# Kernel tuning notes

Hardware: AMD Instinct MI355X
Metric: run time of the kernel (lower is better)

## Reference

```python
import jax, jax.numpy as jnp
import numpy as np

HEADS = 16
HEAD_DIM = 64

def setup_inputs() -> dict:
    key = jax.random.key(0)
    ks = jax.random.split(key, 5)
    S, B, H = 1024, 4, 1024
    scale = 1.0 / np.sqrt(H)
    return {
        "hidden_states": jax.random.normal(ks[0], (S, B, H), jnp.float32),
        "attention_mask": jnp.zeros((B * HEADS, 1, S), jnp.float32),
        "Wq": jax.random.normal(ks[1], (H, H), jnp.float32) * scale,
        "bq": jnp.zeros((H,), jnp.float32),
        "Wk": jax.random.normal(ks[2], (H, H), jnp.float32) * scale,
        "bk": jnp.zeros((H,), jnp.float32),
        "Wv": jax.random.normal(ks[3], (H, H), jnp.float32) * scale,
        "bv": jnp.zeros((H,), jnp.float32),
    }

def reference(hidden_states, attention_mask, Wq, bq, Wk, bk, Wv, bv):
    S, B, H = hidden_states.shape
    d = HEAD_DIM
    inv_sqrt_d = 1.0 / np.sqrt(d)
    # QKV projections (torch Linear: x @ W.T + b)
    q = hidden_states @ Wq.T + bq  # (S, B, H)
    k = hidden_states @ Wk.T + bk
    v = hidden_states @ Wv.T + bv
    # (S, B*heads, d) -> (B*heads, S, d)
    q = q.reshape(S, B * HEADS, d).transpose(1, 0, 2)
    k = k.reshape(S, B * HEADS, d).transpose(1, 0, 2)
    v = v.reshape(S, B * HEADS, d).transpose(1, 0, 2)
    # SDDMM: scaled scores + additive mask -> (B*heads, S, S)
    scores = jnp.einsum('nsd,ntd->nst', q, k) * inv_sqrt_d + attention_mask
    probs = jax.nn.softmax(scores, axis=-1)
    # AV bmm -> (B*heads, S, d); note: dropout in source is seeded but never applied
    ctx = jnp.einsum('nst,ntd->nsd', probs, v)
    # back to (S, B, hidden)
    ctx = ctx.transpose(1, 0, 2).reshape(S, B, H)
    return ctx
```

## Files before the change

kernel.cpp:

```cpp
#include <hip/hip_runtime.h>
#include <hip/hip_bf16.h>
#include <math.h>

#define S_LEN 1024
#define BATCH 4
#define HID 1024
#define NHEADS 16
#define DHEAD 64
#define NTOT 64
#define M_ROWS 4096

typedef unsigned short u16;
typedef unsigned int u32;
typedef __bf16 bf16x8 __attribute__((ext_vector_type(8)));
typedef float f32x4 __attribute__((ext_vector_type(4)));

__device__ __forceinline__ u16 f2bf(float x) {
    __hip_bfloat16 h = __float2bfloat16(x);
    return *(u16*)&h;
}

__device__ __forceinline__ float fexp2(float x) {
#if __has_builtin(__builtin_amdgcn_exp2f)
    return __builtin_amdgcn_exp2f(x);
#else
    return __expf(x * 0.6931471805599453f);
#endif
}

__device__ __forceinline__ u32 cvtpk(float a, float b) {
    u32 r;
    asm("v_cvt_pk_bf16_f32 %0, %1, %2" : "=v"(r) : "v"(a), "v"(b));
    return r;
}

__device__ __forceinline__ void pl16swap(u32& a, u32& b) {
    asm("v_permlane16_swap_b32 %0, %1" : "+v"(a), "+v"(b));
}

__device__ __forceinline__ void gll16(const u16* g, u16* l) {
    __builtin_amdgcn_global_load_lds(
        (const __attribute__((address_space(1))) u32*)g,
        (__attribute__((address_space(3))) u32*)l, 16, 0, 0);
}

__global__ __launch_bounds__(256) void cvt_all(
    const float* __restrict__ X, const float* __restrict__ wq,
    const float* __restrict__ wk, const float* __restrict__ wv,
    u16* __restrict__ Xb, u16* __restrict__ Wb)
{
    const int bid = blockIdx.x;
    const float* src;
    u16* dst;
    size_t off;
    if (bid < 4096) {
        src = X; dst = Xb; off = (size_t)bid * 1024;
    } else {
        const int wb = bid - 4096;
        const int which = wb >> 10;
        src = (which == 0) ? wq : (which == 1) ? wk : wv;
        dst = Wb + (size_t)which * HID * HID;
        off = (size_t)(wb & 1023) * 1024;
    }
    const size_t idx = off + threadIdx.x * 4;
    float4 x = *(const float4*)(src + idx);
    *(ushort4*)(dst + idx) = make_ushort4(f2bf(x.x), f2bf(x.y), f2bf(x.z), f2bf(x.w));
}

__global__ __launch_bounds__(256, 3) void qkv_mfma(
    const u16* __restrict__ Xb, const u16* __restrict__ Wb,
    const float* __restrict__ bq, const float* __restrict__ bk,
    const float* __restrict__ bv,
    u16* __restrict__ Qb, u16* __restrict__ Kb, u16* __restrict__ VT)
{
    const int m0 = blockIdx.x * 128;
    const int n0 = blockIdx.y * 128;
    const int which = blockIdx.z;

    __shared__ __align__(16) u16 As[128 * 64];
    __shared__ __align__(16) u16 Bs[128 * 64];

    const int tid = threadIdx.x;
    const int lane = tid & 63;
    const int w = tid >> 6;
    const int wm = w & 1, wn = w >> 1;
    const int quad = lane >> 4;
    const int l15 = lane & 15;
    const int r7 = l15 & 7;

    const u16* W = Wb + (size_t)which * HID * HID;

    f32x4 acc[4][4];
    #pragma unroll
    for (int i = 0; i < 4; ++i)
        #pragma unroll
        for (int j = 0; j < 4; ++j)
            #pragma unroll
            for (int r = 0; r < 4; ++r) acc[i][j][r] = 0.0f;

    const int srow = lane >> 3;
    const int scg  = ((lane & 7) ^ srow) * 8;

    for (int k0 = 0; k0 < HID; k0 += 64) {
        #pragma unroll
        for (int c = 0; c < 4; ++c) {
            const int seg = w * 4 + c;
            const int row = seg * 8 + srow;
            gll16(Xb + (size_t)(m0 + row) * HID + k0 + scg, As + seg * 512);
            gll16(W  + (size_t)(n0 + row) * HID + k0 + scg, Bs + seg * 512);
        }
        __syncthreads();

        #pragma unroll
        for (int kk = 0; kk < 2; ++kk) {
            const int xo = ((kk * 4 + quad) ^ r7) * 8;
            bf16x8 af[4], bf[4];
            #pragma unroll
            for (int i = 0; i < 4; ++i)
                af[i] = *(const bf16x8*)(As + (wm * 64 + i * 16 + l15) * 64 + xo);
            #pragma unroll
            for (int j = 0; j < 4; ++j)
                bf[j] = *(const bf16x8*)(Bs + (wn * 64 + j * 16 + l15) * 64 + xo);
            #pragma unroll
            for (int i = 0; i < 4; ++i)
                #pragma unroll
                for (int j = 0; j < 4; ++j)
                    acc[i][j] = __builtin_amdgcn_mfma_f32_16x16x32_bf16(
                        af[i], bf[j], acc[i][j], 0, 0, 0);
        }
        __syncthreads();
    }

    const float* bias = (which == 0) ? bq : (which == 1) ? bk : bv;
    #pragma unroll
    for (int j = 0; j < 4; ++j) {
        const int o = n0 + wn * 64 + j * 16 + l15;
        const float bias_v = bias[o];
        const int head = o >> 6, d = o & 63;
        #pragma unroll
        for (int i = 0; i < 4; ++i) {
            const int mbase = m0 + wm * 64 + i * 16 + quad * 4;
            const int s = mbase >> 2;
            #pragma unroll
            for (int r = 0; r < 4; ++r) {
                const int n = r * NHEADS + head;
                const u16 hv = f2bf(acc[i][j][r] + bias_v);
                if (which == 0)
                    Qb[((size_t)n * S_LEN + s) * DHEAD + d] = hv;
                else if (which == 1)
                    Kb[((size_t)n * S_LEN + s) * DHEAD + d] = hv;
                else
                    VT[(size_t)n * (DHEAD * S_LEN) + (size_t)d * S_LEN + s] = hv;
            }
        }
    }
}

__global__ __launch_bounds__(256, 2) void attn_mfma(
    const u16* __restrict__ Qb, const u16* __restrict__ Kb,
    const u16* __restrict__ VT, const float* __restrict__ mask,
    float* __restrict__ out)
{
    const int bid = blockIdx.x;
    const int swz = (bid & 7) * 64 + (bid >> 3);
    const int n = swz >> 3;
    const int s0 = (swz & 7) * 128;
    const int b = n >> 4, head = n & 15;

    __shared__ __align__(16) char smem[36864];
    u16* Kbuf = (u16*)smem;
    u16* Vbuf = (u16*)(smem + 16384);
    float* Ms = (float*)(smem + 32768);
    float* Of = (float*)smem;

    const int tid = threadIdx.x;
    const int lane = tid & 63;
    const int w = tid >> 6;
    const int quad = lane >> 4;
    const int l15 = lane & 15;
    const int r7 = l15 & 7;
    const size_t nbase = (size_t)n * S_LEN * DHEAD;

    const float LOG2E = 1.44269504f;
    const float SCL2  = 0.18033688f;
    const float MOFF  = -23.0831099f;

    const int xs0 = ((quad ^ r7) * 8);
    const int xs1 = (((4 + quad) ^ r7) * 8);
    const int qperm = ((quad & 1) << 1) | (quad >> 1);
    const int xv0 = ((qperm ^ r7) * 8);
    const int xv1 = (((4 + qperm) ^ r7) * 8);

    const int srow = lane >> 3;
    const int scg  = (lane & 7) ^ (srow & 7);

    {
        float4 mv = *(const float4*)(mask + (size_t)n * S_LEN + tid * 4);
        Ms[tid * 4 + 0] = fmaf(mv.x, LOG2E, MOFF);
        Ms[tid * 4 + 1] = fmaf(mv.y, LOG2E, MOFF);
        Ms[tid * 4 + 2] = fmaf(mv.z, LOG2E, MOFF);
        Ms[tid * 4 + 3] = fmaf(mv.w, LOG2E, MOFF);
    }

    bf16x8 qf[2][2];
    #pragma unroll
    for (int mi = 0; mi < 2; ++mi)
        #pragma unroll
        for (int st = 0; st < 2; ++st)
            qf[mi][st] = *(const bf16x8*)(Qb + nbase +
                (size_t)(s0 + w * 32 + mi * 16 + l15) * 64 + st * 32 + quad * 8);

    f32x4 O[2][4];
    float l_lane[2];
    #pragma unroll
    for (int mi = 0; mi < 2; ++mi) {
        l_lane[mi] = 0.0f;
        #pragma unroll
        for (int jt = 0; jt < 4; ++jt)
            #pragma unroll
            for (int r = 0; r < 4; ++r) O[mi][jt][r] = 0.0f;
    }

    {
        #pragma unroll
        for (int c = 0; c < 2; ++c) {
            const int seg = w * 2 + c;
            const int row = seg * 8 + srow;
            gll16(Kb + nbase + (size_t)row * 64 + scg * 8, Kbuf + seg * 512);
            gll16(VT + nbase + (size_t)row * S_LEN + scg * 8, Vbuf + seg * 512);
        }
    }
    __syncthreads();

    for (int it = 0; it < 16; ++it) {
        const int t0 = it * 64;
        const u16* kb = Kbuf + (it & 1) * 4096;
        const u16* vb = Vbuf + (it & 1) * 4096;

        if (it < 15) {
            u16* kd = Kbuf + ((it + 1) & 1) * 4096;
            u16* vd = Vbuf + ((it + 1) & 1) * 4096;
            #pragma unroll
            for (int c = 0; c < 2; ++c) {
                const int seg = w * 2 + c;
                const int row = seg * 8 + srow;
                gll16(Kb + nbase + (size_t)(t0 + 64 + row) * 64 + scg * 8, kd + seg * 512);
                gll16(VT + nbase + (size_t)row * S_LEN + t0 + 64 + scg * 8, vd + seg * 512);
            }
        }

        f32x4 sc[2][4];
        #pragma unroll
        for (int mi = 0; mi < 2; ++mi)
            #pragma unroll
            for (int j = 0; j < 4; ++j)
                #pragma unroll
                for (int r = 0; r < 4; ++r) sc[mi][j][r] = 0.0f;

        __builtin_amdgcn_s_setprio(1);
        #pragma unroll
        for (int st = 0; st < 2; ++st) {
            const int xo = st ? xs1 : xs0;
            bf16x8 kf[4];
            #pragma unroll
            for (int j = 0; j < 4; ++j)
                kf[j] = *(const bf16x8*)(kb + (j * 16 + l15) * 64 + xo);
            #pragma unroll
            for (int mi = 0; mi < 2; ++mi)
                #pragma unroll
                for (int j = 0; j < 4; ++j)
                    sc[mi][j] = __builtin_amdgcn_mfma_f32_16x16x32_bf16(
                        kf[j], qf[mi][st], sc[mi][j], 0, 0, 0);
        }
        __builtin_amdgcn_s_setprio(0);

        float4 mb4[4];
        #pragma unroll
        for (int j = 0; j < 4; ++j)
            mb4[j] = *(const float4*)(Ms + t0 + j * 16 + quad * 4);

        u32 pw[2][2][4];
        #pragma unroll
        for (int mi = 0; mi < 2; ++mi) {
            float pj[4][4];
            #pragma unroll
            for (int j = 0; j < 4; ++j) {
                pj[j][0] = fexp2(fmaf(sc[mi][j][0], SCL2, mb4[j].x));
                pj[j][1] = fexp2(fmaf(sc[mi][j][1], SCL2, mb4[j].y));
                pj[j][2] = fexp2(fmaf(sc[mi][j][2], SCL2, mb4[j].z));
                pj[j][3] = fexp2(fmaf(sc[mi][j][3], SCL2, mb4[j].w));
                l_lane[mi] += (pj[j][0] + pj[j][1]) + (pj[j][2] + pj[j][3]);
            }
            u32 W00 = cvtpk(pj[0][0], pj[0][1]), W01 = cvtpk(pj[0][2], pj[0][3]);
            u32 W10 = cvtpk(pj[1][0], pj[1][1]), W11 = cvtpk(pj[1][2], pj[1][3]);
            u32 W20 = cvtpk(pj[2][0], pj[2][1]), W21 = cvtpk(pj[2][2], pj[2][3]);
            u32 W30 = cvtpk(pj[3][0], pj[3][1]), W31 = cvtpk(pj[3][2], pj[3][3]);
            pl16swap(W00, W10); pl16swap(W01, W11);
            pl16swap(W20, W30); pl16swap(W21, W31);
            pw[mi][0][0] = W00; pw[mi][0][1] = W01;
            pw[mi][0][2] = W10; pw[mi][0][3] = W11;
            pw[mi][1][0] = W20; pw[mi][1][1] = W21;
            pw[mi][1][2] = W30; pw[mi][1][3] = W31;
        }

        __builtin_amdgcn_s_setprio(1);
        #pragma unroll
        for (int st = 0; st < 2; ++st) {
            const int xo = st ? xv1 : xv0;
            bf16x8 vf[4];
            #pragma unroll
            for (int jt = 0; jt < 4; ++jt)
                vf[jt] = *(const bf16x8*)(vb + (jt * 16 + l15) * 64 + xo);
            #pragma unroll
            for (int mi = 0; mi < 2; ++mi) {
                union { u32 wds[4]; bf16x8 v; } pu;
                pu.wds[0] = pw[mi][st][0]; pu.wds[1] = pw[mi][st][1];
                pu.wds[2] = pw[mi][st][2]; pu.wds[3] = pw[mi][st][3];
                #pragma unroll
                for (int jt = 0; jt < 4; ++jt)
                    O[mi][jt] = __builtin_amdgcn_mfma_f32_16x16x32_bf16(
                        vf[jt], pu.v, O[mi][jt], 0, 0, 0);
            }
        }
        __builtin_amdgcn_s_setprio(0);

        __syncthreads();
    }

    float inv_l[2];
    #pragma unroll
    for (int mi = 0; mi < 2; ++mi) {
        float l = l_lane[mi];
        l += __shfl_xor(l, 16);
        l += __shfl_xor(l, 32);
        inv_l[mi] = 1.0f / l;
    }
    __syncthreads();

    #pragma unroll
    for (int mi = 0; mi < 2; ++mi) {
        const int q = w * 32 + mi * 16 + l15;
        #pragma unroll
        for (int jt = 0; jt < 4; ++jt)
            #pragma unroll
            for (int r = 0; r < 4; ++r)
                Of[q * 72 + jt * 16 + quad * 4 + r] = O[mi][jt][r] * inv_l[mi];
    }
    __syncthreads();

    const int tx = tid & 15, ty = tid >> 4;
    #pragma unroll
    for (int p = 0; p < 8; ++p) {
        const int q = p * 16 + ty;
        float4 v = *(const float4*)(Of + q * 72 + tx * 4);
        *(float4*)(out + (size_t)(s0 + q) * (BATCH * HID) + (size_t)b * HID +
                   head * DHEAD + tx * 4) = v;
    }
}

extern "C" void kernel_launch(void* const* d_in, const int* in_sizes, int n_in,
                              void* d_out, int out_size, void* d_ws, size_t ws_size,
                              hipStream_t stream)
{
    const float* X    = (const float*)d_in[0];
    const float* mask = (const float*)d_in[1];
    const float* Wq   = (const float*)d_in[2];
    const float* bq   = (const float*)d_in[3];
    const float* Wk   = (const float*)d_in[4];
    const float* bk   = (const float*)d_in[5];
    const float* Wv   = (const float*)d_in[6];
    const float* bv   = (const float*)d_in[7];
    float* out = (float*)d_out;

    const size_t MX = (size_t)M_ROWS * HID;
    const size_t MW = (size_t)HID * HID;
    u16* wsp = (u16*)d_ws;
    u16* Xb = wsp;
    u16* Wb = Xb + MX;
    u16* Qb = Wb + 3 * MW;
    u16* Kb = Qb + MX;
    u16* VT = Kb + MX;

    cvt_all<<<dim3(4096 + 3072), 256, 0, stream>>>(X, Wq, Wk, Wv, Xb, Wb);
    qkv_mfma<<<dim3(M_ROWS / 128, HID / 128, 3), 256, 0, stream>>>(
        Xb, Wb, bq, bk, bv, Qb, Kb, VT);
    attn_mfma<<<dim3(S_LEN / 128 * NTOT), 256, 0, stream>>>(Qb, Kb, VT, mask, out);
}
```

Baseline: 146.5 us.

## Process 128-key tiles per iteration to halve barrier count in attention loop

The attention kernel's KV loop now covers 128 keys per iteration as two 64-key halves instead of one 64-key tile, with double-buffered K/V shared memory doubled to 64 KB. This halves the number of __syncthreads barriers and async-load rounds. The two halves' exp/pack results are held in registers before the PV MFMAs. The larger LDS footprint (about 68 KB per block) and extra live registers may reduce occupancy below the 2 blocks per CU requested in launch bounds.

```diff
diff --git a/kernel.cpp b/kernel.cpp
--- a/kernel.cpp
+++ b/kernel.cpp
@@ -167,10 +167,10 @@
     const int s0 = (swz & 7) * 128;
     const int b = n >> 4, head = n & 15;
 
-    __shared__ __align__(16) char smem[36864];
+    __shared__ __align__(16) char smem[69632];
     u16* Kbuf = (u16*)smem;
-    u16* Vbuf = (u16*)(smem + 16384);
-    float* Ms = (float*)(smem + 32768);
+    u16* Vbuf = (u16*)(smem + 32768);
+    float* Ms = (float*)(smem + 65536);
     float* Of = (float*)smem;
 
     const int tid = threadIdx.x;
@@ -223,103 +223,124 @@
 
     {
         #pragma unroll
-        for (int c = 0; c < 2; ++c) {
-            const int seg = w * 2 + c;
-            const int row = seg * 8 + srow;
-            gll16(Kb + nbase + (size_t)row * 64 + scg * 8, Kbuf + seg * 512);
-            gll16(VT + nbase + (size_t)row * S_LEN + scg * 8, Vbuf + seg * 512);
-        }
-    }
-    __syncthreads();
-
-    for (int it = 0; it < 16; ++it) {
-        const int t0 = it * 64;
-        const u16* kb = Kbuf + (it & 1) * 4096;
-        const u16* vb = Vbuf + (it & 1) * 4096;
-
-        if (it < 15) {
-            u16* kd = Kbuf + ((it + 1) & 1) * 4096;
-            u16* vd = Vbuf + ((it + 1) & 1) * 4096;
+        for (int h = 0; h < 2; ++h) {
             #pragma unroll
             for (int c = 0; c < 2; ++c) {
                 const int seg = w * 2 + c;
                 const int row = seg * 8 + srow;
-                gll16(Kb + nbase + (size_t)(t0 + 64 + row) * 64 + scg * 8, kd + seg * 512);
-                gll16(VT + nbase + (size_t)row * S_LEN + t0 + 64 + scg * 8, vd + seg * 512);
-            }
-        }
-
-        f32x4 sc[2][4];
-        #pragma unroll
-        for (int mi = 0; mi < 2; ++mi)
+                gll16(Kb + nbase + (size_t)(h * 64 + row) * 64 + scg * 8,
+                      Kbuf + h * 4096 + seg * 512);
+                gll16(VT + nbase + (size_t)row * S_LEN + h * 64 + scg * 8,
+                      Vbuf + h * 4096 + seg * 512);
+            }
+        }
+    }
+    __syncthreads();
+
+    u32 pw[2][2][2][4];
+
+    for (int it = 0; it < 8; ++it) {
+        const int t0 = it * 128;
+        const u16* kb = Kbuf + (it & 1) * 8192;
+        const u16* vb = Vbuf + (it & 1) * 8192;
+
+        if (it < 7) {
+            u16* kd = Kbuf + ((it + 1) & 1) * 8192;
+            u16* vd = Vbuf + ((it + 1) & 1) * 8192;
+            const int t0n = t0 + 128;
+            #pragma unroll
+            for (int h = 0; h < 2; ++h) {
+                #pragma unroll
+                for (int c = 0; c < 2; ++c) {
+                    const int seg = w * 2 + c;
+                    const int row = seg * 8 + srow;
+                    gll16(Kb + nbase + (size_t)(t0n + h * 64 + row) * 64 + scg * 8,
+                          kd + h * 4096 + seg * 512);
+                    gll16(VT + nbase + (size_t)row * S_LEN + t0n + h * 64 + scg * 8,
+                          vd + h * 4096 + seg * 512);
+                }
+            }
+        }
+
+        #pragma unroll
+        for (int h = 0; h < 2; ++h) {
+            const u16* kbh = kb + h * 4096;
+
+            f32x4 sc[2][4];
+            #pragma unroll
+            for (int mi = 0; mi < 2; ++mi)
+                #pragma unroll
+                for (int j = 0; j < 4; ++j)
+                    #pragma unroll
+                    for (int r = 0; r < 4; ++r) sc[mi][j][r] = 0.0f;
+
+            __builtin_amdgcn_s_setprio(1);
+            #pragma unroll
+            for (int st = 0; st < 2; ++st) {
+                const int xo = st ? xs1 : xs0;
+                bf16x8 kf[4];
+                #pragma unroll
+                for (int j = 0; j < 4; ++j)
+                    kf[j] = *(const bf16x8*)(kbh + (j * 16 + l15) * 64 + xo);
+                #pragma unroll
+                for (int mi = 0; mi < 2; ++mi)
+                    #pragma unroll
+                    for (int j = 0; j < 4; ++j)
+                        sc[mi][j] = __builtin_amdgcn_mfma_f32_16x16x32_bf16(
+                            kf[j], qf[mi][st], sc[mi][j], 0, 0, 0);
+            }
+            __builtin_amdgcn_s_setprio(0);
+
+            float4 mb4[4];
             #pragma unroll
             for (int j = 0; j < 4; ++j)
-                #pragma unroll
-                for (int r = 0; r < 4; ++r) sc[mi][j][r] = 0.0f;
+                mb4[j] = *(const float4*)(Ms + t0 + h * 64 + j * 16 + quad * 4);
+
+            #pragma unroll
+            for (int mi = 0; mi < 2; ++mi) {
+                float pj[4][4];
+                #pragma unroll
+                for (int j = 0; j < 4; ++j) {
+                    pj[j][0] = fexp2(fmaf(sc[mi][j][0], SCL2, mb4[j].x));
+                    pj[j][1] = fexp2(fmaf(sc[mi][j][1], SCL2, mb4[j].y));
+                    pj[j][2] = fexp2(fmaf(sc[mi][j][2], SCL2, mb4[j].z));
+                    pj[j][3] = fexp2(fmaf(sc[mi][j][3], SCL2, mb4[j].w));
+                    l_lane[mi] += (pj[j][0] + pj[j][1]) + (pj[j][2] + pj[j][3]);
+                }
+                u32 W00 = cvtpk(pj[0][0], pj[0][1]), W01 = cvtpk(pj[0][2], pj[0][3]);
+                u32 W10 = cvtpk(pj[1][0], pj[1][1]), W11 = cvtpk(pj[1][2], pj[1][3]);
+                u32 W20 = cvtpk(pj[2][0], pj[2][1]), W21 = cvtpk(pj[2][2], pj[2][3]);
+                u32 W30 = cvtpk(pj[3][0], pj[3][1]), W31 = cvtpk(pj[3][2], pj[3][3]);
+                pl16swap(W00, W10); pl16swap(W01, W11);
+                pl16swap(W20, W30); pl16swap(W21, W31);
+                pw[mi][h][0][0] = W00; pw[mi][h][0][1] = W01;
+                pw[mi][h][0][2] = W10; pw[mi][h][0][3] = W11;
+                pw[mi][h][1][0] = W20; pw[mi][h][1][1] = W21;
+                pw[mi][h][1][2] = W30; pw[mi][h][1][3] = W31;
+            }
+        }
 
         __builtin_amdgcn_s_setprio(1);
         #pragma unroll
-        for (int st = 0; st < 2; ++st) {
-            const int xo = st ? xs1 : xs0;
-            bf16x8 kf[4];
-            #pragma unroll
-            for (int j = 0; j < 4; ++j)
-                kf[j] = *(const bf16x8*)(kb + (j * 16 + l15) * 64 + xo);
-            #pragma unroll
-            for (int mi = 0; mi < 2; ++mi)
-                #pragma unroll
-                for (int j = 0; j < 4; ++j)
-                    sc[mi][j] = __builtin_amdgcn_mfma_f32_16x16x32_bf16(
-                        kf[j], qf[mi][st], sc[mi][j], 0, 0, 0);
-        }
-        __builtin_amdgcn_s_setprio(0);
-
-        float4 mb4[4];
-        #pragma unroll
-        for (int j = 0; j < 4; ++j)
-            mb4[j] = *(const float4*)(Ms + t0 + j * 16 + quad * 4);
-
-        u32 pw[2][2][4];
-        #pragma unroll
-        for (int mi = 0; mi < 2; ++mi) {
-            float pj[4][4];
-            #pragma unroll
-            for (int j = 0; j < 4; ++j) {
-                pj[j][0] = fexp2(fmaf(sc[mi][j][0], SCL2, mb4[j].x));
-                pj[j][1] = fexp2(fmaf(sc[mi][j][1], SCL2, mb4[j].y));
-                pj[j][2] = fexp2(fmaf(sc[mi][j][2], SCL2, mb4[j].z));
-                pj[j][3] = fexp2(fmaf(sc[mi][j][3], SCL2, mb4[j].w));
-                l_lane[mi] += (pj[j][0] + pj[j][1]) + (pj[j][2] + pj[j][3]);
-            }
-            u32 W00 = cvtpk(pj[0][0], pj[0][1]), W01 = cvtpk(pj[0][2], pj[0][3]);
-            u32 W10 = cvtpk(pj[1][0], pj[1][1]), W11 = cvtpk(pj[1][2], pj[1][3]);
-            u32 W20 = cvtpk(pj[2][0], pj[2][1]), W21 = cvtpk(pj[2][2], pj[2][3]);
-            u32 W30 = cvtpk(pj[3][0], pj[3][1]), W31 = cvtpk(pj[3][2], pj[3][3]);
-            pl16swap(W00, W10); pl16swap(W01, W11);
-            pl16swap(W20, W30); pl16swap(W21, W31);
-            pw[mi][0][0] = W00; pw[mi][0][1] = W01;
-            pw[mi][0][2] = W10; pw[mi][0][3] = W11;
-            pw[mi][1][0] = W20; pw[mi][1][1] = W21;
-            pw[mi][1][2] = W30; pw[mi][1][3] = W31;
-        }
-
-        __builtin_amdgcn_s_setprio(1);
-        #pragma unroll
-        for (int st = 0; st < 2; ++st) {
-            const int xo = st ? xv1 : xv0;
-            bf16x8 vf[4];
-            #pragma unroll
-            for (int jt = 0; jt < 4; ++jt)
-                vf[jt] = *(const bf16x8*)(vb + (jt * 16 + l15) * 64 + xo);
-            #pragma unroll
-            for (int mi = 0; mi < 2; ++mi) {
-                union { u32 wds[4]; bf16x8 v; } pu;
-                pu.wds[0] = pw[mi][st][0]; pu.wds[1] = pw[mi][st][1];
-                pu.wds[2] = pw[mi][st][2]; pu.wds[3] = pw[mi][st][3];
+        for (int h = 0; h < 2; ++h) {
+            const u16* vbh = vb + h * 4096;
+            #pragma unroll
+            for (int st = 0; st < 2; ++st) {
+                const int xo = st ? xv1 : xv0;
+                bf16x8 vf[4];
                 #pragma unroll
                 for (int jt = 0; jt < 4; ++jt)
-                    O[mi][jt] = __builtin_amdgcn_mfma_f32_16x16x32_bf16(
-                        vf[jt], pu.v, O[mi][jt], 0, 0, 0);
+                    vf[jt] = *(const bf16x8*)(vbh + (jt * 16 + l15) * 64 + xo);
+                #pragma unroll
+                for (int mi = 0; mi < 2; ++mi) {
+                    union { u32 wds[4]; bf16x8 v; } pu;
+                    pu.wds[0] = pw[mi][h][st][0]; pu.wds[1] = pw[mi][h][st][1];
+                    pu.wds[2] = pw[mi][h][st][2]; pu.wds[3] = pw[mi][h][st][3];
+                    #pragma unroll
+                    for (int jt = 0; jt < 4; ++jt)
+                        O[mi][jt] = __builtin_amdgcn_mfma_f32_16x16x32_bf16(
+                            vf[jt], pu.v, O[mi][jt], 0, 0, 0);
+                }
             }
         }
         __builtin_amdgcn_s_setprio(0);
```

Measured after the change: 146.1 us (median of 2 runs). Within noise of the previous version (-0.3%).
